# Optimization experiments

Measured on AMD Instinct MI355X. Metric: run time of the kernel, lower is better.

## Reference

```python
import jax, jax.numpy as jnp
import numpy as np
from jax import lax

B, C, H, W = 4, 3, 384, 384
NBOX = 10

KX = jnp.array([[-1., 0., 1.], [-2., 0., 2.], [-1., 0., 1.]], jnp.float32)
KY = jnp.array([[1., 2., 1.], [0., 0., 0.], [-1., -2., -1.]], jnp.float32)


def sobel(x):
    # x: [N, C, H, W]; per-channel 3x3 cross-correlation with zero padding=1,
    # returns |sobel_x| + |sobel_y| (same as Sobelxy.forward, fully batched)
    n, c, h, w = x.shape
    k = jnp.stack([KX, KY])[:, None]  # [2,1,3,3]
    o = lax.conv_general_dilated(x.reshape(n * c, 1, h, w), k, (1, 1), [(1, 1), (1, 1)])
    return (jnp.abs(o[:, 0]) + jnp.abs(o[:, 1])).reshape(n, c, h, w)


def setup_inputs() -> dict:
    key = jax.random.key(0)
    k1, k2, k3, k4 = jax.random.split(key, 4)
    image_vis = jax.random.uniform(k1, (B, C, H, W), jnp.float32)
    image_ir = jax.random.uniform(k2, (B, C, H, W), jnp.float32)
    generate_img = jax.random.uniform(k3, (B, C, H, W), jnp.float32)
    LW_th = jax.random.uniform(k4, (B, C, H, W), jnp.float32)
    # boxes: [cls, x1, y1, x2, y2]; all-zero coords => skipped box
    rng = np.random.default_rng(0)
    x1 = rng.integers(0, W // 2, (B, NBOX))
    x2 = np.minimum(x1 + rng.integers(16, W // 2, (B, NBOX)), W)
    y1 = rng.integers(0, H // 2, (B, NBOX))
    y2 = np.minimum(y1 + rng.integers(16, H // 2, (B, NBOX)), H)
    cls = rng.integers(0, 5, (B, NBOX))
    lab = np.stack([cls, x1, y1, x2, y2], axis=-1)
    lab[:, 6:, :] = 0  # ragged: only 6 real boxes per batch
    label = jnp.asarray(lab, jnp.int32)
    return dict(b=jnp.float32(0.7), c=jnp.float32(0.4), image_vis=image_vis,
                image_ir=image_ir, generate_img=generate_img, label=label, LW_th=LW_th)


def reference(b, c, image_vis, image_ir, generate_img, label, LW_th):
    alpha, beta = b, c
    vis, ir, th, gen = image_vis, image_ir, LW_th, generate_img
    Bn, Cn, Hn, Wn = vis.shape

    x_in_mean = 0.5 * vis + 0.5 * th
    x_in_mean_7 = 0.3 * vis + 0.7 * th
    x_in_mean_max = jnp.maximum(vis, x_in_mean)

    y_grad = sobel(vis)
    mean_grad = sobel(x_in_mean)
    gen_grad = sobel(gen)
    x_grad_joint = jnp.maximum(y_grad, mean_grad)

    loss_in = 0.5 * jnp.mean(jnp.abs(gen - x_in_mean_max), axis=(1, 2, 3))
    loss_grad = jnp.mean(jnp.abs(gen_grad - x_grad_joint), axis=(1, 2, 3))
    loss_MSE = 0.25 * jnp.mean((gen - vis) ** 2, axis=(1, 2, 3)) + \
               0.25 * jnp.mean((gen - ir) ** 2, axis=(1, 2, 3))
    loss_global = alpha * (loss_in + loss_MSE) + (1.0 - alpha) * loss_grad

    # --- per-object ragged losses via box masks (jit-friendly) ---
    x1 = label[..., 1]; y1 = label[..., 2]; x2 = label[..., 3]; y2 = label[..., 4]  # [B,NBOX]
    valid = (x1 != 0) | (y1 != 0) | (x2 != 0) | (y2 != 0)
    rows = jnp.arange(Hn)[None, None, :, None]
    cols = jnp.arange(Wn)[None, None, None, :]
    mask = ((rows >= y1[:, :, None, None]) & (rows < y2[:, :, None, None]) &
            (cols >= x1[:, :, None, None]) & (cols < x2[:, :, None, None])).astype(vis.dtype)  # [B,NBOX,H,W]
    count = mask.sum((-2, -1))  # pixels per box [B,NBOX]

    # masked image (zeros outside box): sobel of this restricted to the box equals
    # sobel (zero-padded) of the cropped object, matching the original crops
    mv = vis[:, None] * mask[:, :, None]          # [B,NBOX,C,H,W]
    mg = gen[:, None] * mask[:, :, None]
    mm = x_in_mean_7[:, None] * mask[:, :, None]
    gv = sobel(mv.reshape(Bn * NBOX, Cn, Hn, Wn)).reshape(Bn, NBOX, Cn, Hn, Wn)
    gg = sobel(mg.reshape(Bn * NBOX, Cn, Hn, Wn)).reshape(Bn, NBOX, Cn, Hn, Wn)
    gm = sobel(mm.reshape(Bn * NBOX, Cn, Hn, Wn)).reshape(Bn, NBOX, Cn, Hn, Wn)

    grad_max = jnp.maximum(gv, gm)
    in_max = jnp.maximum(mv, mm)
    denom = jnp.maximum(count * Cn, 1.0)
    m5 = mask[:, :, None]
    Lssim = jnp.where(valid, jnp.sum(jnp.abs(gg - grad_max) * m5, axis=(-3, -2, -1)) / denom, 0.0)
    L1loss = jnp.where(valid, jnp.sum(jnp.abs(mg - in_max) * m5, axis=(-3, -2, -1)) / denom, 0.0)

    exist = ((Lssim != 0) | (L1loss != 0)).astype(vis.dtype).sum(-1)  # [B]
    safe = jnp.maximum(exist, 1.0)
    ls = jnp.where(exist > 0, Lssim.sum(-1) / safe, 0.0)
    lin = jnp.where(exist > 0, L1loss.sum(-1) / safe, 0.0)
    loss_label = jnp.where(exist > 0, (1.0 - beta) * ls + beta * lin, 0.0)

    loss_ss = jnp.zeros(Bn, vis.dtype)
    return (loss_ss, loss_global, loss_label, loss_in, loss_grad, ls, lin)
```

## Files before the change

### kernel.cpp

```cpp
#include <hip/hip_runtime.h>

#define Bn 4
#define Cn 3
#define Hn 384
#define Wn 384
#define NBOXn 10

#define CHUNK 1024
#define GBLK  (Bn * Cn * Hn * Wn / CHUNK)
#define BPB   (GBLK / Bn)
#define NACC  23
#define WSTRIDE 24


__device__ __forceinline__ float zp_load(const float* __restrict__ img, int bc, int h, int w) {
    if ((unsigned)h >= (unsigned)Hn || (unsigned)w >= (unsigned)Wn) return 0.0f;
    return img[((size_t)bc * Hn + h) * Wn + w];
}

__device__ __forceinline__ void sobel_xy(const float a[3][3], float& gx, float& gy) {
    gx = (a[0][2] - a[0][0]) + 2.0f * (a[1][2] - a[1][0]) + (a[2][2] - a[2][0]);
    gy = (a[0][0] - a[2][0]) + 2.0f * (a[0][1] - a[2][1]) + (a[0][2] - a[2][2]);
}

__device__ __forceinline__ float waveSum(float x) {
    #pragma unroll
    for (int off = 32; off > 0; off >>= 1) x += __shfl_down(x, off, 64);
    return x;
}

__global__ void __launch_bounds__(256)
fused_loss_kernel(const float* __restrict__ vis,
                  const float* __restrict__ ir,
                  const float* __restrict__ gen,
                  const float* __restrict__ th,
                  const int* __restrict__ label,
                  float* __restrict__ ws) {
    int blk = blockIdx.x;
    int b = blk / BPB;

    int X1[NBOXn], Y1[NBOXn], X2[NBOXn], Y2[NBOXn];
    #pragma unroll
    for (int n = 0; n < NBOXn; n++) {
        const int* lab = label + (b * NBOXn + n) * 5;
        X1[n] = lab[1]; Y1[n] = lab[2]; X2[n] = lab[3]; Y2[n] = lab[4];
    }

    float acc[NACC];
    #pragma unroll
    for (int j = 0; j < NACC; j++) acc[j] = 0.0f;

    int base = blk * CHUNK;
    #pragma unroll 1
    for (int s = 0; s < CHUNK / 256; s++) {
        int idx = base + s * 256 + (int)threadIdx.x;
        int w = idx % Wn;
        int t = idx / Wn;
        int h = t % Hn;
        int bc = t / Hn;

        float av[3][3], at_[3][3], ag[3][3];
        #pragma unroll
        for (int r = 0; r < 3; r++) {
            #pragma unroll
            for (int c = 0; c < 3; c++) {
                int hh = h - 1 + r, wp = w - 1 + c;
                av[r][c]  = zp_load(vis, bc, hh, wp);
                at_[r][c] = zp_load(th,  bc, hh, wp);
                ag[r][c]  = zp_load(gen, bc, hh, wp);
            }
        }
        float v = av[1][1], g = ag[1][1], tc = at_[1][1];
        float irv = ir[idx];

        float gxv, gyv, gxt, gyt, gxg, gyg;
        sobel_xy(av, gxv, gyv);
        sobel_xy(at_, gxt, gyt);
        sobel_xy(ag, gxg, gyg);
        float ygrad = fabsf(gxv) + fabsf(gyv);
        float mgrad = fabsf(0.5f * (gxv + gxt)) + fabsf(0.5f * (gyv + gyt));
        float g7    = fabsf(0.3f * gxv + 0.7f * gxt) + fabsf(0.3f * gyv + 0.7f * gyt);
        float ggrad = fabsf(gxg) + fabsf(gyg);

        float amc  = 0.5f * v + 0.5f * tc;
        float am7c = 0.3f * v + 0.7f * tc;
        acc[0] += fabsf(g - fmaxf(v, amc));
        float dv = g - v, di = g - irv;
        acc[2] += 0.25f * (dv * dv + di * di);
        acc[1] += fabsf(ggrad - fmaxf(ygrad, mgrad));

        float l1c = fabsf(g - fmaxf(v, am7c));

        #pragma unroll
        for (int n = 0; n < NBOXn; n++) {
            bool inb = (w >= X1[n]) & (w < X2[n]) & (h >= Y1[n]) & (h < Y2[n]);
            if (inb) {
                bool interior = (w - 1 >= X1[n]) & (w + 1 < X2[n]) &
                                (h - 1 >= Y1[n]) & (h + 1 < Y2[n]);
                float gvb, gmb, ggb;
                if (interior) {
                    gvb = ygrad; gmb = g7; ggb = ggrad;
                } else {
                    float mv[3][3], mm[3][3], mg[3][3];
                    #pragma unroll
                    for (int r = 0; r < 3; r++) {
                        #pragma unroll
                        for (int c = 0; c < 3; c++) {
                            int hh = h - 1 + r, wp = w - 1 + c;
                            bool ib = (hh >= Y1[n]) & (hh < Y2[n]) & (wp >= X1[n]) & (wp < X2[n]);
                            float fv = ib ? av[r][c]  : 0.0f;
                            float ft = ib ? at_[r][c] : 0.0f;
                            float fg = ib ? ag[r][c]  : 0.0f;
                            mv[r][c] = fv;
                            mg[r][c] = fg;
                            mm[r][c] = 0.3f * fv + 0.7f * ft;
                        }
                    }
                    float a1, a2;
                    sobel_xy(mv, a1, a2); gvb = fabsf(a1) + fabsf(a2);
                    sobel_xy(mm, a1, a2); gmb = fabsf(a1) + fabsf(a2);
                    sobel_xy(mg, a1, a2); ggb = fabsf(a1) + fabsf(a2);
                }
                acc[3 + 2 * n]     += fabsf(ggb - fmaxf(gvb, gmb));
                acc[3 + 2 * n + 1] += l1c;
            }
        }
    }

    __shared__ float red[NACC][4];
    int lane = threadIdx.x & 63, wv = threadIdx.x >> 6;
    #pragma unroll
    for (int j = 0; j < NACC; j++) {
        float sj = waveSum(acc[j]);
        if (lane == 0) red[j][wv] = sj;
    }
    __syncthreads();
    if (threadIdx.x < NACC) {
        int j = threadIdx.x;
        ws[(size_t)blk * WSTRIDE + j] = red[j][0] + red[j][1] + red[j][2] + red[j][3];
    }
}

__global__ void __launch_bounds__(256)
finalize_kernel(const float* __restrict__ alpha_p,
                const float* __restrict__ beta_p,
                const int* __restrict__ label,
                const float* __restrict__ ws,
                float* __restrict__ out) {
    int b = blockIdx.x;
    float a[NACC];
    #pragma unroll
    for (int j = 0; j < NACC; j++) a[j] = 0.0f;

    for (int r = threadIdx.x; r < BPB; r += 256) {
        const float* p = ws + (size_t)(b * BPB + r) * WSTRIDE;
        #pragma unroll
        for (int j = 0; j < NACC; j++) a[j] += p[j];
    }

    __shared__ float red[NACC][4];
    int lane = threadIdx.x & 63, wv = threadIdx.x >> 6;
    #pragma unroll
    for (int j = 0; j < NACC; j++) {
        float sj = waveSum(a[j]);
        if (lane == 0) red[j][wv] = sj;
    }
    __syncthreads();

    if (threadIdx.x == 0) {
        float alpha = *alpha_p, beta = *beta_p;
        const float invN = 1.0f / (float)(Cn * Hn * Wn);

        float loss_in   = 0.5f * (red[0][0] + red[0][1] + red[0][2] + red[0][3]) * invN;
        float loss_grad = (red[1][0] + red[1][1] + red[1][2] + red[1][3]) * invN;
        float loss_mse  = (red[2][0] + red[2][1] + red[2][2] + red[2][3]) * invN;
        float loss_global = alpha * (loss_in + loss_mse) + (1.0f - alpha) * loss_grad;

        float lssim_sum = 0.0f, l1_sum = 0.0f;
        int exist = 0;
        for (int n = 0; n < NBOXn; n++) {
            const int* lab = label + (b * NBOXn + n) * 5;
            int x1 = lab[1], y1 = lab[2], x2 = lab[3], y2 = lab[4];
            bool valid = (x1 | y1 | x2 | y2) != 0;
            float Ls = 0.0f, L1 = 0.0f;
            if (valid) {
                int bw = x2 - x1, bh = y2 - y1;
                int cnt = (bw > 0 && bh > 0) ? bw * bh : 0;
                float denom = fmaxf((float)(cnt * Cn), 1.0f);
                int j0 = 3 + 2 * n;
                Ls = (red[j0][0] + red[j0][1] + red[j0][2] + red[j0][3]) / denom;
                L1 = (red[j0 + 1][0] + red[j0 + 1][1] + red[j0 + 1][2] + red[j0 + 1][3]) / denom;
            }
            if (Ls != 0.0f || L1 != 0.0f) exist++;
            lssim_sum += Ls;
            l1_sum += L1;
        }
        float ls = 0.0f, lin = 0.0f, loss_label = 0.0f;
        if (exist > 0) {
            float safe = (float)exist;
            ls = lssim_sum / safe;
            lin = l1_sum / safe;
            loss_label = (1.0f - beta) * ls + beta * lin;
        }
        out[0 * Bn + b] = 0.0f;
        out[1 * Bn + b] = loss_global;
        out[2 * Bn + b] = loss_label;
        out[3 * Bn + b] = loss_in;
        out[4 * Bn + b] = loss_grad;
        out[5 * Bn + b] = ls;
        out[6 * Bn + b] = lin;
    }
}

extern "C" void kernel_launch(void* const* d_in, const int* in_sizes, int n_in,
                              void* d_out, int out_size, void* d_ws, size_t ws_size,
                              hipStream_t stream) {
    const float* bp    = (const float*)d_in[0];
    const float* cp    = (const float*)d_in[1];
    const float* vis   = (const float*)d_in[2];
    const float* ir    = (const float*)d_in[3];
    const float* gen   = (const float*)d_in[4];
    const int*   label = (const int*)d_in[5];
    const float* th    = (const float*)d_in[6];
    float* out = (float*)d_out;
    float* ws  = (float*)d_ws;

    fused_loss_kernel<<<GBLK, 256, 0, stream>>>(vis, ir, gen, th, label, ws);
    finalize_kernel<<<Bn, 256, 0, stream>>>(bp, cp, label, ws, out);
}
```

Measured before the change: 116.6 us.

## Tile stencil into shared memory with sliding rows and per-tile box culling

Replaces per-pixel 27 global loads with a 2D tile (128x16 plus halo) staged into LDS via float4 loads. Each thread then walks 8 rows, rotating a 3x3 register window. Per-tile box intersection flags let threads skip boxes that miss the tile. The block-to-workspace index mapping is kept consistent with finalize. This trades extra LDS use and a sync for much less redundant global and L2 traffic.

```diff
diff --git a/kernel.cpp b/kernel.cpp
--- a/kernel.cpp
+++ b/kernel.cpp
@@ -6,27 +6,29 @@
 #define Wn 384
 #define NBOXn 10
 
-#define CHUNK 1024
-#define GBLK  (Bn * Cn * Hn * Wn / CHUNK)
-#define BPB   (GBLK / Bn)
-#define NACC  23
+#define TW 128
+#define TH 16
+#define GX (Wn / TW)
+#define GY (Hn / TH)
+#define GZ (Bn * Cn)
+#define GBLK (GX * GY * GZ)
+#define BPB (GBLK / Bn)
+#define NACC 23
 #define WSTRIDE 24
-
-
-__device__ __forceinline__ float zp_load(const float* __restrict__ img, int bc, int h, int w) {
-    if ((unsigned)h >= (unsigned)Hn || (unsigned)w >= (unsigned)Wn) return 0.0f;
-    return img[((size_t)bc * Hn + h) * Wn + w];
+#define LROWS (TH + 2)
+#define LSTR 136
+#define NSEG (LSTR / 4)
+
+
+__device__ __forceinline__ float waveSum(float x) {
+    #pragma unroll
+    for (int off = 32; off > 0; off >>= 1) x += __shfl_down(x, off, 64);
+    return x;
 }
 
 __device__ __forceinline__ void sobel_xy(const float a[3][3], float& gx, float& gy) {
     gx = (a[0][2] - a[0][0]) + 2.0f * (a[1][2] - a[1][0]) + (a[2][2] - a[2][0]);
     gy = (a[0][0] - a[2][0]) + 2.0f * (a[0][1] - a[2][1]) + (a[0][2] - a[2][2]);
-}
-
-__device__ __forceinline__ float waveSum(float x) {
-    #pragma unroll
-    for (int off = 32; off > 0; off >>= 1) x += __shfl_down(x, off, 64);
-    return x;
 }
 
 __global__ void __launch_bounds__(256)
@@ -36,46 +38,90 @@
                   const float* __restrict__ th,
                   const int* __restrict__ label,
                   float* __restrict__ ws) {
-    int blk = blockIdx.x;
-    int b = blk / BPB;
+    __shared__ float sV[LROWS * LSTR];
+    __shared__ float sT[LROWS * LSTR];
+    __shared__ float sG[LROWS * LSTR];
+
+    const int tid = threadIdx.x;
+    const int w0 = blockIdx.x * TW;
+    const int h0 = blockIdx.y * TH;
+    const int bc = blockIdx.z;
+    const int b  = bc / Cn;
+
+    for (int i = tid; i < LROWS * NSEG; i += 256) {
+        int row = i / NSEG, seg = i % NSEG;
+        int h  = h0 - 1 + row;
+        int wf = w0 - 4 + seg * 4;
+        float4 fv, ft, fg;
+        if ((unsigned)h < (unsigned)Hn && wf >= 0 && wf <= Wn - 4) {
+            size_t o = ((size_t)bc * Hn + h) * Wn + wf;
+            fv = *(const float4*)(vis + o);
+            ft = *(const float4*)(th  + o);
+            fg = *(const float4*)(gen + o);
+        } else if ((unsigned)h < (unsigned)Hn) {
+            float* pv = &fv.x; float* pt = &ft.x; float* pg = &fg.x;
+            size_t ro = ((size_t)bc * Hn + h) * Wn;
+            #pragma unroll
+            for (int j = 0; j < 4; j++) {
+                int wj = wf + j;
+                bool in = (unsigned)wj < (unsigned)Wn;
+                pv[j] = in ? vis[ro + wj] : 0.0f;
+                pt[j] = in ? th [ro + wj] : 0.0f;
+                pg[j] = in ? gen[ro + wj] : 0.0f;
+            }
+        } else {
+            fv = make_float4(0.f, 0.f, 0.f, 0.f); ft = fv; fg = fv;
+        }
+        int lo = row * LSTR + seg * 4;
+        *(float4*)&sV[lo] = fv;
+        *(float4*)&sT[lo] = ft;
+        *(float4*)&sG[lo] = fg;
+    }
 
     int X1[NBOXn], Y1[NBOXn], X2[NBOXn], Y2[NBOXn];
+    bool hit[NBOXn];
     #pragma unroll
     for (int n = 0; n < NBOXn; n++) {
         const int* lab = label + (b * NBOXn + n) * 5;
         X1[n] = lab[1]; Y1[n] = lab[2]; X2[n] = lab[3]; Y2[n] = lab[4];
+        hit[n] = (X2[n] > w0) & (X1[n] < w0 + TW) & (Y2[n] > h0) & (Y1[n] < h0 + TH);
     }
 
     float acc[NACC];
     #pragma unroll
     for (int j = 0; j < NACC; j++) acc[j] = 0.0f;
 
-    int base = blk * CHUNK;
+    __syncthreads();
+
+    const int tx  = tid & (TW - 1);
+    const int tyg = tid >> 7;
+    const int ty0 = tyg * (TH / 2);
+    const int cl  = tx + 3;
+    const int w   = w0 + tx;
+
+    float av[3][3], atb[3][3], ag[3][3];
+    #pragma unroll
+    for (int r = 0; r < 2; r++) {
+        int lo = (ty0 + r) * LSTR + cl;
+        av [r][0] = sV[lo]; av [r][1] = sV[lo + 1]; av [r][2] = sV[lo + 2];
+        atb[r][0] = sT[lo]; atb[r][1] = sT[lo + 1]; atb[r][2] = sT[lo + 2];
+        ag [r][0] = sG[lo]; ag [r][1] = sG[lo + 1]; ag [r][2] = sG[lo + 2];
+    }
+
     #pragma unroll 1
-    for (int s = 0; s < CHUNK / 256; s++) {
-        int idx = base + s * 256 + (int)threadIdx.x;
-        int w = idx % Wn;
-        int t = idx / Wn;
-        int h = t % Hn;
-        int bc = t / Hn;
-
-        float av[3][3], at_[3][3], ag[3][3];
-        #pragma unroll
-        for (int r = 0; r < 3; r++) {
-            #pragma unroll
-            for (int c = 0; c < 3; c++) {
-                int hh = h - 1 + r, wp = w - 1 + c;
-                av[r][c]  = zp_load(vis, bc, hh, wp);
-                at_[r][c] = zp_load(th,  bc, hh, wp);
-                ag[r][c]  = zp_load(gen, bc, hh, wp);
-            }
-        }
-        float v = av[1][1], g = ag[1][1], tc = at_[1][1];
-        float irv = ir[idx];
+    for (int k = 0; k < TH / 2; k++) {
+        int lo = (ty0 + k + 2) * LSTR + cl;
+        av [2][0] = sV[lo]; av [2][1] = sV[lo + 1]; av [2][2] = sV[lo + 2];
+        atb[2][0] = sT[lo]; atb[2][1] = sT[lo + 1]; atb[2][2] = sT[lo + 2];
+        ag [2][0] = sG[lo]; ag [2][1] = sG[lo + 1]; ag [2][2] = sG[lo + 2];
+
+        const int h = h0 + ty0 + k;
+        float v = av[1][1], g = ag[1][1], tc = atb[1][1];
+        float irv = ir[((size_t)bc * Hn + h) * Wn + w];
 
         float gxv, gyv, gxt, gyt, gxg, gyg;
         sobel_xy(av, gxv, gyv);
-        sobel_xy(at_, gxt, gyt);
+        sobel_xy(atb, gxt, gyt);
         sobel_xy(ag, gxg, gyg);
         float ygrad = fabsf(gxv) + fabsf(gyv);
         float mgrad = fabsf(0.5f * (gxv + gxt)) + fabsf(0.5f * (gyv + gyt));
@@ -93,51 +139,61 @@
 
         #pragma unroll
         for (int n = 0; n < NBOXn; n++) {
-            bool inb = (w >= X1[n]) & (w < X2[n]) & (h >= Y1[n]) & (h < Y2[n]);
-            if (inb) {
-                bool interior = (w - 1 >= X1[n]) & (w + 1 < X2[n]) &
-                                (h - 1 >= Y1[n]) & (h + 1 < Y2[n]);
-                float gvb, gmb, ggb;
-                if (interior) {
-                    gvb = ygrad; gmb = g7; ggb = ggrad;
-                } else {
-                    float mv[3][3], mm[3][3], mg[3][3];
-                    #pragma unroll
-                    for (int r = 0; r < 3; r++) {
+            if (hit[n]) {
+                bool inb = (w >= X1[n]) & (w < X2[n]) & (h >= Y1[n]) & (h < Y2[n]);
+                if (inb) {
+                    bool interior = (w - 1 >= X1[n]) & (w + 1 < X2[n]) &
+                                    (h - 1 >= Y1[n]) & (h + 1 < Y2[n]);
+                    float gvb, gmb, ggb;
+                    if (interior) {
+                        gvb = ygrad; gmb = g7; ggb = ggrad;
+                    } else {
+                        float mv[3][3], mm[3][3], mg[3][3];
                         #pragma unroll
-                        for (int c = 0; c < 3; c++) {
-                            int hh = h - 1 + r, wp = w - 1 + c;
-                            bool ib = (hh >= Y1[n]) & (hh < Y2[n]) & (wp >= X1[n]) & (wp < X2[n]);
-                            float fv = ib ? av[r][c]  : 0.0f;
-                            float ft = ib ? at_[r][c] : 0.0f;
-                            float fg = ib ? ag[r][c]  : 0.0f;
-                            mv[r][c] = fv;
-                            mg[r][c] = fg;
-                            mm[r][c] = 0.3f * fv + 0.7f * ft;
+                        for (int r = 0; r < 3; r++) {
+                            #pragma unroll
+                            for (int c = 0; c < 3; c++) {
+                                int hh = h - 1 + r, wp = w - 1 + c;
+                                bool ib = (hh >= Y1[n]) & (hh < Y2[n]) &
+                                          (wp >= X1[n]) & (wp < X2[n]);
+                                float fv = ib ? av [r][c] : 0.0f;
+                                float ft = ib ? atb[r][c] : 0.0f;
+                                float fg = ib ? ag [r][c] : 0.0f;
+                                mv[r][c] = fv;
+                                mg[r][c] = fg;
+                                mm[r][c] = 0.3f * fv + 0.7f * ft;
+                            }
                         }
+                        float a1, a2;
+                        sobel_xy(mv, a1, a2); gvb = fabsf(a1) + fabsf(a2);
+                        sobel_xy(mm, a1, a2); gmb = fabsf(a1) + fabsf(a2);
+                        sobel_xy(mg, a1, a2); ggb = fabsf(a1) + fabsf(a2);
                     }
-                    float a1, a2;
-                    sobel_xy(mv, a1, a2); gvb = fabsf(a1) + fabsf(a2);
-                    sobel_xy(mm, a1, a2); gmb = fabsf(a1) + fabsf(a2);
-                    sobel_xy(mg, a1, a2); ggb = fabsf(a1) + fabsf(a2);
+                    acc[3 + 2 * n]     += fabsf(ggb - fmaxf(gvb, gmb));
+                    acc[3 + 2 * n + 1] += l1c;
                 }
-                acc[3 + 2 * n]     += fabsf(ggb - fmaxf(gvb, gmb));
-                acc[3 + 2 * n + 1] += l1c;
             }
         }
+
+        #pragma unroll
+        for (int c = 0; c < 3; c++) {
+            av [0][c] = av [1][c]; av [1][c] = av [2][c];
+            atb[0][c] = atb[1][c]; atb[1][c] = atb[2][c];
+            ag [0][c] = ag [1][c]; ag [1][c] = ag [2][c];
+        }
     }
 
     __shared__ float red[NACC][4];
-    int lane = threadIdx.x & 63, wv = threadIdx.x >> 6;
+    int lane = tid & 63, wv = tid >> 6;
     #pragma unroll
     for (int j = 0; j < NACC; j++) {
         float sj = waveSum(acc[j]);
         if (lane == 0) red[j][wv] = sj;
     }
     __syncthreads();
-    if (threadIdx.x < NACC) {
-        int j = threadIdx.x;
-        ws[(size_t)blk * WSTRIDE + j] = red[j][0] + red[j][1] + red[j][2] + red[j][3];
+    if (tid < NACC) {
+        int blk = (bc * GY + blockIdx.y) * GX + blockIdx.x;
+        ws[(size_t)blk * WSTRIDE + tid] = red[tid][0] + red[tid][1] + red[tid][2] + red[tid][3];
     }
 }
 
@@ -225,6 +281,7 @@
     float* out = (float*)d_out;
     float* ws  = (float*)d_ws;
 
-    fused_loss_kernel<<<GBLK, 256, 0, stream>>>(vis, ir, gen, th, label, ws);
+    dim3 grid(GX, GY, GZ);
+    fused_loss_kernel<<<grid, 256, 0, stream>>>(vis, ir, gen, th, label, ws);
     finalize_kernel<<<Bn, 256, 0, stream>>>(bp, cp, label, ws, out);
 }
```

New measurement: 112.6 us. 1.04x faster.
